# Optimization experiments

Measured on AMD Instinct MI355X. Metric: run time of the kernel, lower is better.

The kernel has to match this reference:

```python
import jax, jax.numpy as jnp
import numpy as np

C = 512
GROUPS = 32
EPS = 1e-6


def group_norm(x, gamma, beta):
    # x: [B,C,H,W]
    b, c, h, w = x.shape
    xg = x.reshape(b, GROUPS, c // GROUPS, h, w)
    mean = xg.mean(axis=(2, 3, 4), keepdims=True)
    var = xg.var(axis=(2, 3, 4), keepdims=True)
    xg = (xg - mean) / jnp.sqrt(var + EPS)
    xn = xg.reshape(b, c, h, w)
    return xn * gamma[None, :, None, None] + beta[None, :, None, None]


def conv1x1(x, w, bias):
    # x: [B,C,H,W], w: [Cout,Cin], bias: [Cout]
    return jnp.einsum('bchw,dc->bdhw', x, w) + bias[None, :, None, None]


def setup_inputs() -> dict:
    key = jax.random.key(0)
    ks = jax.random.split(key, 10)
    scale = 1.0 / np.sqrt(C)
    return {
        'x': jax.random.normal(ks[0], (4, C, 64, 64), dtype=jnp.float32),
        'gn_gamma': jnp.ones((C,), jnp.float32),
        'gn_beta': jnp.zeros((C,), jnp.float32),
        'wq': jax.random.normal(ks[1], (C, C), jnp.float32) * scale,
        'bq': jnp.zeros((C,), jnp.float32),
        'wk': jax.random.normal(ks[2], (C, C), jnp.float32) * scale,
        'bk': jnp.zeros((C,), jnp.float32),
        'wv': jax.random.normal(ks[3], (C, C), jnp.float32) * scale,
        'bv': jnp.zeros((C,), jnp.float32),
        'wp': jax.random.normal(ks[4], (C, C), jnp.float32) * scale,
        'bp': jnp.zeros((C,), jnp.float32),
    }


def reference(x, gn_gamma, gn_beta, wq, bq, wk, bk, wv, bv, wp, bp):
    b, c, h, w = x.shape
    h_ = group_norm(x, gn_gamma, gn_beta)
    q = conv1x1(h_, wq, bq).reshape(b, c, h * w)  # [B,C,N]
    k = conv1x1(h_, wk, bk).reshape(b, c, h * w)
    v = conv1x1(h_, wv, bv).reshape(b, c, h * w)
    # attn[b,i,j] = softmax_j(q_i . k_j / sqrt(c))
    attn = jnp.einsum('bci,bcj->bij', q, k) * (c ** -0.5)  # [B,N,N]
    attn = jax.nn.softmax(attn, axis=2)
    a = jnp.einsum('bij,bcj->bci', attn, v).reshape(b, c, h, w)
    a = conv1x1(a, wp, bp)
    return x + a
```

## Files before the change

### kernel.cpp

```cpp
#include <hip/hip_runtime.h>
#include <hip/hip_bf16.h>

#define B_ 4
#define C_ 512
#define N_ 4096
#define G_ 32
#define CPG_ 16

typedef __bf16 bf16;
using bf16x4 = __attribute__((ext_vector_type(4))) __bf16;
using bf16x8 = __attribute__((ext_vector_type(8))) __bf16;
using f32x4  = __attribute__((ext_vector_type(4))) float;

__global__ __launch_bounds__(256) void gn_stats(const float* __restrict__ x,
                                                float* __restrict__ mv,
                                                float* __restrict__ rv) {
    __shared__ float r1[4], r2[4];
    const int bg = blockIdx.x;
    const float* xg = x + (long)bg * (CPG_ * N_);
    const int tid = threadIdx.x;
    float s = 0.f, ss = 0.f;
    for (int i = tid; i < CPG_ * N_ / 4; i += 256) {
        f32x4 v = ((const f32x4*)xg)[i];
#pragma unroll
        for (int j = 0; j < 4; ++j) { s += v[j]; ss += v[j] * v[j]; }
    }
#pragma unroll
    for (int o = 32; o > 0; o >>= 1) { s += __shfl_down(s, o); ss += __shfl_down(ss, o); }
    if ((tid & 63) == 0) { r1[tid >> 6] = s; r2[tid >> 6] = ss; }
    __syncthreads();
    if (tid == 0) {
        float S = r1[0] + r1[1] + r1[2] + r1[3];
        float SS = r2[0] + r2[1] + r2[2] + r2[3];
        float mean = S / (CPG_ * N_);
        float var = SS / (CPG_ * N_) - mean * mean;
        mv[bg] = mean;
        rv[bg] = rsqrtf(var + 1e-6f);
    }
}

__global__ __launch_bounds__(256) void gn_apply(const float* __restrict__ x,
                                                const float* __restrict__ mv,
                                                const float* __restrict__ rv,
                                                const float* __restrict__ gamma,
                                                const float* __restrict__ beta,
                                                bf16* __restrict__ ht) {
    __shared__ float tile[64][65];
    const int b = blockIdx.z, c0 = blockIdx.y * 64, n0 = blockIdx.x * 64;
    const int tid = threadIdx.x;
    const int rr = tid >> 4, cc4 = (tid & 15) * 4;
    const float* xb = x + ((long)b * C_ + c0) * N_ + n0;
#pragma unroll
    for (int p2 = 0; p2 < 4; ++p2) {
        const int cl = p2 * 16 + rr;
        const int g = (c0 + cl) >> 4;
        const float m = mv[b * G_ + g], rs = rv[b * G_ + g];
        const float ga = gamma[c0 + cl], be = beta[c0 + cl];
        f32x4 v = *(const f32x4*)&xb[(long)cl * N_ + cc4];
#pragma unroll
        for (int j = 0; j < 4; ++j) tile[cl][cc4 + j] = (v[j] - m) * rs * ga + be;
    }
    __syncthreads();
    bf16* hb = ht + ((long)b * N_ + n0) * C_ + c0;
#pragma unroll
    for (int p2 = 0; p2 < 4; ++p2) {
        const int nn = p2 * 16 + rr;
        bf16x4 o4 = { (bf16)tile[cc4 + 0][nn], (bf16)tile[cc4 + 1][nn],
                      (bf16)tile[cc4 + 2][nn], (bf16)tile[cc4 + 3][nn] };
        *(bf16x4*)&hb[(long)nn * C_ + cc4] = o4;
    }
}

__global__ __launch_bounds__(256) void f2b4(const float* __restrict__ w0, const float* __restrict__ w1,
                                            const float* __restrict__ w2, const float* __restrict__ w3,
                                            bf16* __restrict__ o0, bf16* __restrict__ o1,
                                            bf16* __restrict__ o2, bf16* __restrict__ o3, int n4) {
    const float* in = (blockIdx.y == 0) ? w0 : (blockIdx.y == 1) ? w1 : (blockIdx.y == 2) ? w2 : w3;
    bf16* o = (blockIdx.y == 0) ? o0 : (blockIdx.y == 1) ? o1 : (blockIdx.y == 2) ? o2 : o3;
    int i = blockIdx.x * 256 + threadIdx.x;
    if (i < n4) {
        f32x4 v = ((const f32x4*)in)[i];
        bf16x4 r = { (bf16)v[0], (bf16)v[1], (bf16)v[2], (bf16)v[3] };
        ((bf16x4*)o)[i] = r;
    }
}

template <int OUTF32, int BIASMODE , int RESID, int GRIDSWAP,
          int EXPSUM, int INVSUM, int DUAL>
__global__ __launch_bounds__(256, 2)
void gemm_bt(const bf16* __restrict__ A, const bf16* __restrict__ Bt,
             void* __restrict__ outp, const float* __restrict__ bias,
             const float* __restrict__ resid,
             float* __restrict__ rowpart, const float* __restrict__ invsum,
             const bf16* __restrict__ Bt2, const float* __restrict__ bias2,
             void* __restrict__ outp2,
             int M, int N, int K, float scale,
             long aStride, long btStride, long outStride, long residStride) {
    __shared__ __align__(16) bf16 lA[2][128 * 32];
    __shared__ __align__(16) bf16 lB[2][128 * 32];

    const int tid = threadIdx.x;
    const int wid = tid >> 6;
    const int lane = tid & 63;
    const int z = blockIdx.z;
    A += (long)z * aStride;
    Bt += (long)z * btStride;
    int ybn = GRIDSWAP ? blockIdx.y : blockIdx.x;
    if (DUAL) {
        const int half = gridDim.y >> 1;
        if (ybn >= half) { ybn -= half; Bt = Bt2; bias = bias2; outp = outp2; }
    }
    const int bm = (GRIDSWAP ? blockIdx.x : blockIdx.y) * 128;
    const int bn = ybn * 128;
    const int wr = (wid >> 1) * 64;
    const int wc = (wid & 1) * 64;

    f32x4 acc[4][4];
#pragma unroll
    for (int m = 0; m < 4; ++m)
#pragma unroll
        for (int n = 0; n < 4; ++n) acc[m][n] = (f32x4){0.f, 0.f, 0.f, 0.f};

    const int srow = lane >> 2;
    const int skcol = (lane & 3) * 8;
    const int lr = lane >> 4;
    const int lc = lane & 15;

    auto stage = [&](int buf, int k0) {
#pragma unroll
        for (int c = 0; c < 2; ++c) {
            const int chunk = wid * 2 + c;
            const int row = chunk * 16 + srow;
            const bf16* gA = A + (long)(bm + row) * K + (k0 + skcol);
            const bf16* gB = Bt + (long)(bn + row) * K + (k0 + skcol);
            __builtin_amdgcn_global_load_lds(
                (const __attribute__((address_space(1))) void*)gA,
                (__attribute__((address_space(3))) void*)&lA[buf][chunk * 512], 16, 0, 0);
            __builtin_amdgcn_global_load_lds(
                (const __attribute__((address_space(1))) void*)gB,
                (__attribute__((address_space(3))) void*)&lB[buf][chunk * 512], 16, 0, 0);
        }
    };

    const int nk = K >> 5;
    stage(0, 0);
    __syncthreads();
    for (int i = 0; i < nk; ++i) {
        if (i + 1 < nk) stage((i + 1) & 1, (i + 1) << 5);
        const int cur = i & 1;
        bf16x8 aF[4], bF[4];
#pragma unroll
        for (int m = 0; m < 4; ++m)
            aF[m] = *(const bf16x8*)&lA[cur][(wr + m * 16 + lc) * 32 + lr * 8];
#pragma unroll
        for (int n = 0; n < 4; ++n)
            bF[n] = *(const bf16x8*)&lB[cur][(wc + n * 16 + lc) * 32 + lr * 8];
#pragma unroll
        for (int m = 0; m < 4; ++m)
#pragma unroll
            for (int n = 0; n < 4; ++n)
                acc[m][n] = __builtin_amdgcn_mfma_f32_16x16x32_bf16(aF[m], bF[n],
                                                                    acc[m][n], 0, 0, 0);
        __syncthreads();
    }

    if constexpr (EXPSUM) {
        __shared__ float rsum[2][128];
        bf16* outB = (bf16*)outp + (long)z * outStride;
        float s_mj[4][4];
#pragma unroll
        for (int m = 0; m < 4; ++m)
#pragma unroll
            for (int j = 0; j < 4; ++j) s_mj[m][j] = 0.f;
#pragma unroll
        for (int m = 0; m < 4; ++m)
#pragma unroll
            for (int n = 0; n < 4; ++n) {
                const int gc = bn + wc + n * 16 + lc;
#pragma unroll
                for (int j = 0; j < 4; ++j) {
                    const int gr = bm + wr + m * 16 + lr * 4 + j;
                    float e = __expf(fminf(acc[m][n][j] * scale, 60.f));
                    outB[(long)gr * N + gc] = (bf16)e;
                    s_mj[m][j] += e;
                }
            }
#pragma unroll
        for (int m = 0; m < 4; ++m)
#pragma unroll
            for (int j = 0; j < 4; ++j)
#pragma unroll
                for (int o = 1; o < 16; o <<= 1)
                    s_mj[m][j] += __shfl_xor(s_mj[m][j], o);
        if (lc == 0) {
#pragma unroll
            for (int m = 0; m < 4; ++m)
#pragma unroll
                for (int j = 0; j < 4; ++j)
                    rsum[wc >> 6][wr + m * 16 + lr * 4 + j] = s_mj[m][j];
        }
        __syncthreads();
        if (tid < 128) {
            float p = rsum[0][tid] + rsum[1][tid];
            rowpart[((long)z * M + bm + tid) * gridDim.x + blockIdx.x] = p;
        }
        return;
    }

    float invs[4][4];
    if constexpr (INVSUM) {
#pragma unroll
        for (int m = 0; m < 4; ++m)
#pragma unroll
            for (int j = 0; j < 4; ++j)
                invs[m][j] = invsum[(long)z * M + bm + wr + m * 16 + lr * 4 + j];
    }

    float* outF = (float*)outp + (long)z * outStride;
    bf16* outB = (bf16*)outp + (long)z * outStride;
    const float* res = resid + (long)z * residStride;
#pragma unroll
    for (int m = 0; m < 4; ++m) {
#pragma unroll
        for (int n = 0; n < 4; ++n) {
            const int gc = bn + wc + n * 16 + lc;
            float cb = (BIASMODE == 1) ? bias[gc] : 0.f;
#pragma unroll
            for (int j = 0; j < 4; ++j) {
                const int gr = bm + wr + m * 16 + lr * 4 + j;
                float v = INVSUM ? acc[m][n][j] * invs[m][j]
                                 : acc[m][n][j] * scale + cb;
                if (BIASMODE == 2) v += bias[gr];
                long idx = (long)gr * N + gc;
                if (RESID) v += res[idx];
                if (OUTF32) outF[idx] = v;
                else        outB[idx] = (bf16)v;
            }
        }
    }
}

__global__ __launch_bounds__(256) void rowinv(const float* __restrict__ rowpart,
                                              float* __restrict__ invsum, int nblk) {
    const int row = blockIdx.x * 256 + threadIdx.x;
    const float* rp = rowpart + (long)row * nblk;
    float s = 0.f;
    for (int i = 0; i < nblk; ++i) s += rp[i];
    invsum[row] = 1.f / s;
}

extern "C" void kernel_launch(void* const* d_in, const int* in_sizes, int n_in,
                              void* d_out, int out_size, void* d_ws, size_t ws_size,
                              hipStream_t stream) {
    const float* x     = (const float*)d_in[0];
    const float* gamma = (const float*)d_in[1];
    const float* beta  = (const float*)d_in[2];
    const float* wq = (const float*)d_in[3]; const float* bq = (const float*)d_in[4];
    const float* wk = (const float*)d_in[5]; const float* bk = (const float*)d_in[6];
    const float* wv = (const float*)d_in[7]; const float* bv = (const float*)d_in[8];
    const float* wp = (const float*)d_in[9]; const float* bp = (const float*)d_in[10];

    char* w = (char*)d_ws;
    size_t off = 0;
    auto take = [&](size_t bytes) -> void* {
        void* pp = w + off;
        off += (bytes + 255) & ~(size_t)255;
        return pp;
    };
    float* mv = (float*)take(B_ * G_ * 4);
    float* rv = (float*)take(B_ * G_ * 4);
    bf16* wqb = (bf16*)take((size_t)C_ * C_ * 2);
    bf16* wkb = (bf16*)take((size_t)C_ * C_ * 2);
    bf16* wvb = (bf16*)take((size_t)C_ * C_ * 2);
    bf16* wpb = (bf16*)take((size_t)C_ * C_ * 2);
    bf16* ht  = (bf16*)take((size_t)B_ * N_ * C_ * 2);
    bf16* qt  = (bf16*)take((size_t)B_ * N_ * C_ * 2);
    bf16* kt  = (bf16*)take((size_t)B_ * N_ * C_ * 2);
    bf16* vv  = (bf16*)take((size_t)B_ * C_ * N_ * 2);
    bf16* at  = ht;
    float* rowpart = (float*)take((size_t)B_ * N_ * 32 * 4);
    float* invsum  = (float*)take((size_t)B_ * N_ * 4);

    const bool tierA = ws_size >= 205587456ULL;

    gn_stats<<<dim3(B_ * G_), 256, 0, stream>>>(x, mv, rv);
    gn_apply<<<dim3(N_ / 64, C_ / 64, B_), 256, 0, stream>>>(x, mv, rv, gamma, beta, ht);
    f2b4<<<dim3(C_ * C_ / 4 / 256, 4), 256, 0, stream>>>(wq, wk, wv, wp, wqb, wkb, wvb, wpb,
                                                         C_ * C_ / 4);

    gemm_bt<0, 1, 0, 1, 0, 0, 1><<<dim3(B_ * N_ / 128, 2 * C_ / 128, 1), 256, 0, stream>>>(
        ht, wqb, qt, bq, nullptr, nullptr, nullptr, wkb, bk, kt,
        B_ * N_, C_, C_, 1.f, 0, 0, 0, 0);
    gemm_bt<0, 2, 0, 0, 0, 0, 0><<<dim3(N_ / 128, C_ / 128, B_), 256, 0, stream>>>(
        wvb, ht, vv, bv, nullptr, nullptr, nullptr, nullptr, nullptr, nullptr,
        C_, N_, C_, 1.f, 0, (long)N_ * C_, (long)C_ * N_, 0);

    const float scl = 0.044194173824159216f;
    if (tierA) {
        bf16* sc = (bf16*)take((size_t)B_ * N_ * N_ * 2);
        gemm_bt<0, 0, 0, 0, 1, 0, 0><<<dim3(N_ / 128, N_ / 128, B_), 256, 0, stream>>>(
            qt, kt, sc, nullptr, nullptr, rowpart, nullptr, nullptr, nullptr, nullptr,
            N_, N_, C_, scl, (long)N_ * C_, (long)N_ * C_, (long)N_ * N_, 0);
        rowinv<<<dim3(B_ * N_ / 256), 256, 0, stream>>>(rowpart, invsum, N_ / 128);
        gemm_bt<0, 0, 0, 1, 0, 1, 0><<<dim3(N_ / 128, C_ / 128, B_), 256, 0, stream>>>(
            sc, vv, at, nullptr, nullptr, nullptr, invsum, nullptr, nullptr, nullptr,
            N_, C_, N_, 1.f, (long)N_ * N_, (long)C_ * N_, (long)N_ * C_, 0);
    } else {
        bf16* sc = (bf16*)take((size_t)2 * N_ * N_ * 2);
        for (int p = 0; p < 2; ++p) {
            const long o2 = (long)p * 2 * N_ * C_;
            gemm_bt<0, 0, 0, 0, 1, 0, 0><<<dim3(N_ / 128, N_ / 128, 2), 256, 0, stream>>>(
                qt + o2, kt + o2, sc, nullptr, nullptr, rowpart, nullptr, nullptr,
                nullptr, nullptr, N_, N_, C_, scl,
                (long)N_ * C_, (long)N_ * C_, (long)N_ * N_, 0);
            rowinv<<<dim3(2 * N_ / 256), 256, 0, stream>>>(rowpart, invsum, N_ / 128);
            gemm_bt<0, 0, 0, 1, 0, 1, 0><<<dim3(N_ / 128, C_ / 128, 2), 256, 0, stream>>>(
                sc, vv + o2, at + o2, nullptr, nullptr, nullptr, invsum, nullptr,
                nullptr, nullptr, N_, C_, N_, 1.f,
                (long)N_ * N_, (long)C_ * N_, (long)N_ * C_, 0);
        }
    }
    gemm_bt<1, 2, 1, 0, 0, 0, 0><<<dim3(N_ / 128, C_ / 128, B_), 256, 0, stream>>>(
        wpb, at, d_out, bp, x, nullptr, nullptr, nullptr, nullptr, nullptr,
        C_, N_, C_, 1.f, 0, (long)N_ * C_, (long)C_ * N_, (long)C_ * N_);
}
```

Before: 396.6 us.

## Parameterize GEMM tile shape, shrink tiles for small grids, split GroupNorm stats

Templates the bf16 MFMA GEMM on per-wave tile counts and an optional double buffer. The V projection, PV and output-projection GEMMs move to 64x128 tiles so they launch more blocks and fill the GPU, and some of them drop double buffering. GroupNorm statistics are split over 8 segments per group, with the final reduction folded into gn_apply, to raise parallelism in the stats pass. The tier selection now derives the workspace requirement from the actual offsets. Smaller tiles lower per-block reuse, and the single-buffered paths add a sync per k-step.

```diff
diff --git a/kernel.cpp b/kernel.cpp
--- a/kernel.cpp
+++ b/kernel.cpp
@@ -12,15 +12,14 @@
 using bf16x8 = __attribute__((ext_vector_type(8))) __bf16;
 using f32x4  = __attribute__((ext_vector_type(4))) float;
 
-__global__ __launch_bounds__(256) void gn_stats(const float* __restrict__ x,
-                                                float* __restrict__ mv,
-                                                float* __restrict__ rv) {
+__global__ __launch_bounds__(256) void gn_stats_part(const float* __restrict__ x,
+                                                     float2* __restrict__ pp) {
     __shared__ float r1[4], r2[4];
-    const int bg = blockIdx.x;
-    const float* xg = x + (long)bg * (CPG_ * N_);
+    const int bg = blockIdx.y, seg = blockIdx.x;
+    const float* xg = x + (long)bg * (CPG_ * N_) + (long)seg * (CPG_ * N_ / 8);
     const int tid = threadIdx.x;
     float s = 0.f, ss = 0.f;
-    for (int i = tid; i < CPG_ * N_ / 4; i += 256) {
+    for (int i = tid; i < CPG_ * N_ / 8 / 4; i += 256) {
         f32x4 v = ((const f32x4*)xg)[i];
 #pragma unroll
         for (int j = 0; j < 4; ++j) { s += v[j]; ss += v[j] * v[j]; }
@@ -30,31 +29,42 @@
     if ((tid & 63) == 0) { r1[tid >> 6] = s; r2[tid >> 6] = ss; }
     __syncthreads();
     if (tid == 0) {
-        float S = r1[0] + r1[1] + r1[2] + r1[3];
-        float SS = r2[0] + r2[1] + r2[2] + r2[3];
-        float mean = S / (CPG_ * N_);
-        float var = SS / (CPG_ * N_) - mean * mean;
-        mv[bg] = mean;
-        rv[bg] = rsqrtf(var + 1e-6f);
+        float2 out;
+        out.x = r1[0] + r1[1] + r1[2] + r1[3];
+        out.y = r2[0] + r2[1] + r2[2] + r2[3];
+        pp[bg * 8 + seg] = out;
     }
 }
 
 __global__ __launch_bounds__(256) void gn_apply(const float* __restrict__ x,
-                                                const float* __restrict__ mv,
-                                                const float* __restrict__ rv,
+                                                const float2* __restrict__ pp,
                                                 const float* __restrict__ gamma,
                                                 const float* __restrict__ beta,
                                                 bf16* __restrict__ ht) {
     __shared__ float tile[64][65];
+    __shared__ float sm[4], srs[4];
     const int b = blockIdx.z, c0 = blockIdx.y * 64, n0 = blockIdx.x * 64;
     const int tid = threadIdx.x;
     const int rr = tid >> 4, cc4 = (tid & 15) * 4;
+    if (tid < 4) {
+        const int g = (c0 >> 4) + tid;
+        float s = 0.f, ss = 0.f;
+#pragma unroll
+        for (int u = 0; u < 8; ++u) {
+            float2 t = pp[(b * G_ + g) * 8 + u];
+            s += t.x; ss += t.y;
+        }
+        const float mean = s / (CPG_ * N_);
+        const float var = ss / (CPG_ * N_) - mean * mean;
+        sm[tid] = mean;
+        srs[tid] = rsqrtf(var + 1e-6f);
+    }
+    __syncthreads();
     const float* xb = x + ((long)b * C_ + c0) * N_ + n0;
 #pragma unroll
     for (int p2 = 0; p2 < 4; ++p2) {
         const int cl = p2 * 16 + rr;
-        const int g = (c0 + cl) >> 4;
-        const float m = mv[b * G_ + g], rs = rv[b * G_ + g];
+        const float m = sm[cl >> 4], rs = srs[cl >> 4];
         const float ga = gamma[c0 + cl], be = beta[c0 + cl];
         f32x4 v = *(const f32x4*)&xb[(long)cl * N_ + cc4];
 #pragma unroll
@@ -85,8 +95,8 @@
     }
 }
 
-template <int OUTF32, int BIASMODE , int RESID, int GRIDSWAP,
-          int EXPSUM, int INVSUM, int DUAL>
+template <int WRM, int WCN, int OUTF32, int BIASMODE ,
+          int RESID, int GRIDSWAP, int EXPSUM, int INVSUM, int DUAL, int DBUF>
 __global__ __launch_bounds__(256, 2)
 void gemm_bt(const bf16* __restrict__ A, const bf16* __restrict__ Bt,
              void* __restrict__ outp, const float* __restrict__ bias,
@@ -96,8 +106,11 @@
              void* __restrict__ outp2,
              int M, int N, int K, float scale,
              long aStride, long btStride, long outStride, long residStride) {
-    __shared__ __align__(16) bf16 lA[2][128 * 32];
-    __shared__ __align__(16) bf16 lB[2][128 * 32];
+    constexpr int BM = 32 * WRM, BN = 32 * WCN;
+    constexpr int CHA = BM / 16, CHB = BN / 16, TOT = CHA + CHB;
+    static_assert(TOT % 4 == 0, "chunk count must divide across 4 waves");
+    __shared__ __align__(16) bf16 lA[DBUF + 1][BM * 32];
+    __shared__ __align__(16) bf16 lB[DBUF + 1][BN * 32];
 
     const int tid = threadIdx.x;
     const int wid = tid >> 6;
@@ -110,16 +123,16 @@
         const int half = gridDim.y >> 1;
         if (ybn >= half) { ybn -= half; Bt = Bt2; bias = bias2; outp = outp2; }
     }
-    const int bm = (GRIDSWAP ? blockIdx.x : blockIdx.y) * 128;
-    const int bn = ybn * 128;
-    const int wr = (wid >> 1) * 64;
-    const int wc = (wid & 1) * 64;
-
-    f32x4 acc[4][4];
-#pragma unroll
-    for (int m = 0; m < 4; ++m)
-#pragma unroll
-        for (int n = 0; n < 4; ++n) acc[m][n] = (f32x4){0.f, 0.f, 0.f, 0.f};
+    const int bm = (GRIDSWAP ? blockIdx.x : blockIdx.y) * BM;
+    const int bn = ybn * BN;
+    const int wr = (wid >> 1) * 16 * WRM;
+    const int wc = (wid & 1) * 16 * WCN;
+
+    f32x4 acc[WRM][WCN];
+#pragma unroll
+    for (int m = 0; m < WRM; ++m)
+#pragma unroll
+        for (int n = 0; n < WCN; ++n) acc[m][n] = (f32x4){0.f, 0.f, 0.f, 0.f};
 
     const int srow = lane >> 2;
     const int skcol = (lane & 3) * 8;
@@ -128,54 +141,71 @@
 
     auto stage = [&](int buf, int k0) {
 #pragma unroll
-        for (int c = 0; c < 2; ++c) {
-            const int chunk = wid * 2 + c;
-            const int row = chunk * 16 + srow;
-            const bf16* gA = A + (long)(bm + row) * K + (k0 + skcol);
-            const bf16* gB = Bt + (long)(bn + row) * K + (k0 + skcol);
-            __builtin_amdgcn_global_load_lds(
-                (const __attribute__((address_space(1))) void*)gA,
-                (__attribute__((address_space(3))) void*)&lA[buf][chunk * 512], 16, 0, 0);
-            __builtin_amdgcn_global_load_lds(
-                (const __attribute__((address_space(1))) void*)gB,
-                (__attribute__((address_space(3))) void*)&lB[buf][chunk * 512], 16, 0, 0);
+        for (int u = 0; u < TOT / 4; ++u) {
+            const int c = wid + u * 4;
+            if (c < CHA) {
+                const int row = c * 16 + srow;
+                const bf16* gA = A + (long)(bm + row) * K + (k0 + skcol);
+                __builtin_amdgcn_global_load_lds(
+                    (const __attribute__((address_space(1))) void*)gA,
+                    (__attribute__((address_space(3))) void*)&lA[buf][c * 512], 16, 0, 0);
+            } else {
+                const int c2 = c - CHA;
+                const int row = c2 * 16 + srow;
+                const bf16* gB = Bt + (long)(bn + row) * K + (k0 + skcol);
+                __builtin_amdgcn_global_load_lds(
+                    (const __attribute__((address_space(1))) void*)gB,
+                    (__attribute__((address_space(3))) void*)&lB[buf][c2 * 512], 16, 0, 0);
+            }
         }
     };
 
-    const int nk = K >> 5;
-    stage(0, 0);
-    __syncthreads();
-    for (int i = 0; i < nk; ++i) {
-        if (i + 1 < nk) stage((i + 1) & 1, (i + 1) << 5);
-        const int cur = i & 1;
-        bf16x8 aF[4], bF[4];
-#pragma unroll
-        for (int m = 0; m < 4; ++m)
+    auto compute = [&](int cur) {
+        bf16x8 aF[WRM], bF[WCN];
+#pragma unroll
+        for (int m = 0; m < WRM; ++m)
             aF[m] = *(const bf16x8*)&lA[cur][(wr + m * 16 + lc) * 32 + lr * 8];
 #pragma unroll
-        for (int n = 0; n < 4; ++n)
+        for (int n = 0; n < WCN; ++n)
             bF[n] = *(const bf16x8*)&lB[cur][(wc + n * 16 + lc) * 32 + lr * 8];
 #pragma unroll
-        for (int m = 0; m < 4; ++m)
-#pragma unroll
-            for (int n = 0; n < 4; ++n)
+        for (int m = 0; m < WRM; ++m)
+#pragma unroll
+            for (int n = 0; n < WCN; ++n)
                 acc[m][n] = __builtin_amdgcn_mfma_f32_16x16x32_bf16(aF[m], bF[n],
                                                                     acc[m][n], 0, 0, 0);
+    };
+
+    const int nk = K >> 5;
+    if (DBUF) {
+        stage(0, 0);
         __syncthreads();
+        for (int i = 0; i < nk; ++i) {
+            if (i + 1 < nk) stage((i + 1) & 1, (i + 1) << 5);
+            compute(i & 1);
+            __syncthreads();
+        }
+    } else {
+        for (int i = 0; i < nk; ++i) {
+            stage(0, i << 5);
+            __syncthreads();
+            compute(0);
+            __syncthreads();
+        }
     }
 
     if constexpr (EXPSUM) {
-        __shared__ float rsum[2][128];
+        __shared__ float rsum[2][BM];
         bf16* outB = (bf16*)outp + (long)z * outStride;
-        float s_mj[4][4];
-#pragma unroll
-        for (int m = 0; m < 4; ++m)
+        float s_mj[WRM][4];
+#pragma unroll
+        for (int m = 0; m < WRM; ++m)
 #pragma unroll
             for (int j = 0; j < 4; ++j) s_mj[m][j] = 0.f;
 #pragma unroll
-        for (int m = 0; m < 4; ++m)
-#pragma unroll
-            for (int n = 0; n < 4; ++n) {
+        for (int m = 0; m < WRM; ++m)
+#pragma unroll
+            for (int n = 0; n < WCN; ++n) {
                 const int gc = bn + wc + n * 16 + lc;
 #pragma unroll
                 for (int j = 0; j < 4; ++j) {
@@ -186,7 +216,7 @@
                 }
             }
 #pragma unroll
-        for (int m = 0; m < 4; ++m)
+        for (int m = 0; m < WRM; ++m)
 #pragma unroll
             for (int j = 0; j < 4; ++j)
 #pragma unroll
@@ -194,23 +224,23 @@
                     s_mj[m][j] += __shfl_xor(s_mj[m][j], o);
         if (lc == 0) {
 #pragma unroll
-            for (int m = 0; m < 4; ++m)
+            for (int m = 0; m < WRM; ++m)
 #pragma unroll
                 for (int j = 0; j < 4; ++j)
-                    rsum[wc >> 6][wr + m * 16 + lr * 4 + j] = s_mj[m][j];
+                    rsum[wid & 1][wr + m * 16 + lr * 4 + j] = s_mj[m][j];
         }
         __syncthreads();
-        if (tid < 128) {
+        if (tid < BM) {
             float p = rsum[0][tid] + rsum[1][tid];
             rowpart[((long)z * M + bm + tid) * gridDim.x + blockIdx.x] = p;
         }
         return;
     }
 
-    float invs[4][4];
+    float invs[WRM][4];
     if constexpr (INVSUM) {
 #pragma unroll
-        for (int m = 0; m < 4; ++m)
+        for (int m = 0; m < WRM; ++m)
 #pragma unroll
             for (int j = 0; j < 4; ++j)
                 invs[m][j] = invsum[(long)z * M + bm + wr + m * 16 + lr * 4 + j];
@@ -220,9 +250,9 @@
     bf16* outB = (bf16*)outp + (long)z * outStride;
     const float* res = resid + (long)z * residStride;
 #pragma unroll
-    for (int m = 0; m < 4; ++m) {
-#pragma unroll
-        for (int n = 0; n < 4; ++n) {
+    for (int m = 0; m < WRM; ++m) {
+#pragma unroll
+        for (int n = 0; n < WCN; ++n) {
             const int gc = bn + wc + n * 16 + lc;
             float cb = (BIASMODE == 1) ? bias[gc] : 0.f;
 #pragma unroll
@@ -267,8 +297,7 @@
         off += (bytes + 255) & ~(size_t)255;
         return pp;
     };
-    float* mv = (float*)take(B_ * G_ * 4);
-    float* rv = (float*)take(B_ * G_ * 4);
+    float2* pp = (float2*)take((size_t)B_ * G_ * 8 * sizeof(float2));
     bf16* wqb = (bf16*)take((size_t)C_ * C_ * 2);
     bf16* wkb = (bf16*)take((size_t)C_ * C_ * 2);
     bf16* wvb = (bf16*)take((size_t)C_ * C_ * 2);
@@ -281,46 +310,53 @@
     float* rowpart = (float*)take((size_t)B_ * N_ * 32 * 4);
     float* invsum  = (float*)take((size_t)B_ * N_ * 4);
 
-    const bool tierA = ws_size >= 205587456ULL;
-
-    gn_stats<<<dim3(B_ * G_), 256, 0, stream>>>(x, mv, rv);
-    gn_apply<<<dim3(N_ / 64, C_ / 64, B_), 256, 0, stream>>>(x, mv, rv, gamma, beta, ht);
+    const bool tierA = (off + (size_t)B_ * N_ * N_ * 2 + 256) <= ws_size;
+
+    gn_stats_part<<<dim3(8, B_ * G_), 256, 0, stream>>>(x, pp);
+    gn_apply<<<dim3(N_ / 64, C_ / 64, B_), 256, 0, stream>>>(x, pp, gamma, beta, ht);
     f2b4<<<dim3(C_ * C_ / 4 / 256, 4), 256, 0, stream>>>(wq, wk, wv, wp, wqb, wkb, wvb, wpb,
                                                          C_ * C_ / 4);
 
-    gemm_bt<0, 1, 0, 1, 0, 0, 1><<<dim3(B_ * N_ / 128, 2 * C_ / 128, 1), 256, 0, stream>>>(
+    gemm_bt<4, 4, 0, 1, 0, 1, 0, 0, 1, 0>
+        <<<dim3(B_ * N_ / 128, 2 * C_ / 128, 1), 256, 0, stream>>>(
         ht, wqb, qt, bq, nullptr, nullptr, nullptr, wkb, bk, kt,
         B_ * N_, C_, C_, 1.f, 0, 0, 0, 0);
-    gemm_bt<0, 2, 0, 0, 0, 0, 0><<<dim3(N_ / 128, C_ / 128, B_), 256, 0, stream>>>(
+    gemm_bt<2, 4, 0, 2, 0, 0, 0, 0, 0, 0>
+        <<<dim3(N_ / 128, C_ / 64, B_), 256, 0, stream>>>(
         wvb, ht, vv, bv, nullptr, nullptr, nullptr, nullptr, nullptr, nullptr,
         C_, N_, C_, 1.f, 0, (long)N_ * C_, (long)C_ * N_, 0);
 
     const float scl = 0.044194173824159216f;
     if (tierA) {
         bf16* sc = (bf16*)take((size_t)B_ * N_ * N_ * 2);
-        gemm_bt<0, 0, 0, 0, 1, 0, 0><<<dim3(N_ / 128, N_ / 128, B_), 256, 0, stream>>>(
+        gemm_bt<4, 4, 0, 0, 0, 0, 1, 0, 0, 1>
+            <<<dim3(N_ / 128, N_ / 128, B_), 256, 0, stream>>>(
             qt, kt, sc, nullptr, nullptr, rowpart, nullptr, nullptr, nullptr, nullptr,
             N_, N_, C_, scl, (long)N_ * C_, (long)N_ * C_, (long)N_ * N_, 0);
         rowinv<<<dim3(B_ * N_ / 256), 256, 0, stream>>>(rowpart, invsum, N_ / 128);
-        gemm_bt<0, 0, 0, 1, 0, 1, 0><<<dim3(N_ / 128, C_ / 128, B_), 256, 0, stream>>>(
+        gemm_bt<2, 4, 0, 0, 0, 1, 0, 1, 0, 1>
+            <<<dim3(N_ / 64, C_ / 128, B_), 256, 0, stream>>>(
             sc, vv, at, nullptr, nullptr, nullptr, invsum, nullptr, nullptr, nullptr,
             N_, C_, N_, 1.f, (long)N_ * N_, (long)C_ * N_, (long)N_ * C_, 0);
     } else {
         bf16* sc = (bf16*)take((size_t)2 * N_ * N_ * 2);
         for (int p = 0; p < 2; ++p) {
             const long o2 = (long)p * 2 * N_ * C_;
-            gemm_bt<0, 0, 0, 0, 1, 0, 0><<<dim3(N_ / 128, N_ / 128, 2), 256, 0, stream>>>(
+            gemm_bt<4, 4, 0, 0, 0, 0, 1, 0, 0, 1>
+                <<<dim3(N_ / 128, N_ / 128, 2), 256, 0, stream>>>(
                 qt + o2, kt + o2, sc, nullptr, nullptr, rowpart, nullptr, nullptr,
                 nullptr, nullptr, N_, N_, C_, scl,
                 (long)N_ * C_, (long)N_ * C_, (long)N_ * N_, 0);
             rowinv<<<dim3(2 * N_ / 256), 256, 0, stream>>>(rowpart, invsum, N_ / 128);
-            gemm_bt<0, 0, 0, 1, 0, 1, 0><<<dim3(N_ / 128, C_ / 128, 2), 256, 0, stream>>>(
+            gemm_bt<2, 4, 0, 0, 0, 1, 0, 1, 0, 1>
+                <<<dim3(N_ / 64, C_ / 128, 2), 256, 0, stream>>>(
                 sc, vv + o2, at + o2, nullptr, nullptr, nullptr, invsum, nullptr,
                 nullptr, nullptr, N_, C_, N_, 1.f,
                 (long)N_ * N_, (long)C_ * N_, (long)N_ * C_, 0);
         }
     }
-    gemm_bt<1, 2, 1, 0, 0, 0, 0><<<dim3(N_ / 128, C_ / 128, B_), 256, 0, stream>>>(
+    gemm_bt<2, 4, 1, 2, 1, 0, 0, 0, 0, 0>
+        <<<dim3(N_ / 128, C_ / 64, B_), 256, 0, stream>>>(
         wpb, at, d_out, bp, x, nullptr, nullptr, nullptr, nullptr, nullptr,
         C_, N_, C_, 1.f, 0, (long)N_ * C_, (long)C_ * N_, (long)C_ * N_);
 }
```

Result: faster. 376.7 us (-5.0%).
